# Kernel tuning notes

Measured on AMD Instinct MI355X. Metric: run time of the kernel, lower is better.

Reference implementation:

```python
import jax, jax.numpy as jnp
import numpy as np

B, P, K, F, H = 128, 200, 60, 4, 64   # events, points/event, knn k, feat dim, hidden
N = B * P


def setup_inputs() -> dict:
    key = jax.random.key(0)
    k0, k1, k2, k3 = jax.random.split(key, 4)
    x = jax.random.normal(k0, (N, F), jnp.float32)
    pos = jax.random.normal(k1, (N, 3), jnp.float32)
    batch = jnp.arange(N, dtype=jnp.int32) // P  # sorted event ids, equal-size events
    W1 = jax.random.normal(k2, (F + 3, H), jnp.float32) / np.sqrt(F + 3)
    b1 = jnp.zeros((H,), jnp.float32)
    W2 = jax.random.normal(k3, (H, H), jnp.float32) / np.sqrt(H)
    b2 = jnp.zeros((H,), jnp.float32)
    return {"x": x, "pos": pos, "batch": batch, "W1": W1, "b1": b1, "W2": W2, "b2": b2}


def _knn_edges(pos):
    """knn_graph(pos, K, batch, loop=False, flow='source_to_target').
    Equal-size events -> batched [B,P,P] pairwise distances, no cross-event edges."""
    p = pos.reshape(B, P, 3)
    d2 = jnp.sum((p[:, :, None, :] - p[:, None, :, :]) ** 2, axis=-1)  # [B,P,P]
    d2 = d2 + jnp.eye(P, dtype=d2.dtype) * 1e10                        # exclude self (loop=False)
    _, nbr = jax.lax.top_k(-d2, K)                                     # [B,P,K] local neighbor ids
    src = (nbr + (jnp.arange(B, dtype=nbr.dtype) * P)[:, None, None]).reshape(-1)  # sources j
    dst = jnp.repeat(jnp.arange(N, dtype=src.dtype), K)                             # targets i
    return jnp.stack([src, dst])  # [2, N*K]


def _local_nn(m, W1, b1, W2, b2):
    h = jax.nn.relu(m @ W1 + b1)
    return jax.nn.relu(h @ W2 + b2)


def reference(x, pos, batch, W1, b1, W2, b2):
    edge_index = _knn_edges(pos)
    src, dst = edge_index[0], edge_index[1]
    # PointConv message: net(concat[x_j, pos_j - pos_i]) on each edge
    rel = pos[src] - pos[dst]                             # [E,3]
    m = jnp.concatenate([x[src], rel], axis=-1)           # [E,F+3]
    h = _local_nn(m, W1, b1, W2, b2)                      # [E,H]
    out = h.reshape(N, K, H).max(axis=1)                  # max-aggregate per target node
    # PyG PointConv adds self-loops by default: message with rel = 0
    m_self = jnp.concatenate([x, jnp.zeros((N, 3), x.dtype)], axis=-1)
    h_self = _local_nn(m_self, W1, b1, W2, b2)            # [N,H]
    out = jnp.maximum(out, h_self)
    return (out, pos, batch, edge_index)
```

## Files before the change

### kernel.cpp

```cpp
#include <hip/hip_runtime.h>
#include <hip/hip_bf16.h>

typedef unsigned int u32;
typedef unsigned long long u64;
typedef __attribute__((ext_vector_type(8))) short bf16x8;
typedef __attribute__((ext_vector_type(4))) float f32x4;
typedef __attribute__((ext_vector_type(4))) u32 u32x4;

#define NB 128
#define PP 200
#define KK 60
#define NN (NB*PP)
#define HH 64

#define OUT_OFF   0
#define POS_OFF   (NN*HH)
#define BATCH_OFF (POS_OFF + NN*3)
#define ESRC_OFF  (BATCH_OFF + NN)
#define EDST_OFF  (ESRC_OFF + NN*KK)

static __device__ __forceinline__ u32 packtr(float a, float b) {
    return __builtin_amdgcn_perm(__float_as_uint(b), __float_as_uint(a), 0x07060302u);
}
static __device__ __forceinline__ u32 prefix_lt(u64 b) {
    return __builtin_amdgcn_mbcnt_hi((u32)(b >> 32),
                                     __builtin_amdgcn_mbcnt_lo((u32)b, 0));
}

__global__ __launch_bounds__(256) void fused_kernel(const float* __restrict__ x,
                                                    const float* __restrict__ pos,
                                                    const float* __restrict__ W1,
                                                    const float* __restrict__ b1p,
                                                    const float* __restrict__ W2,
                                                    const float* __restrict__ b2p,
                                                    float* __restrict__ out) {
    __shared__ alignas(16) float xs[PP * 4];
    __shared__ alignas(16) float psl[PP * 3];
    __shared__ alignas(16) u32 jslot[4 * 128];
    __shared__ alignas(16) u32 msg[4 * 256];
    __shared__ alignas(16) u32 pkW1[64 * 4];
    __shared__ alignas(16) u32 pkW2T[64 * 33];
    __shared__ alignas(16) float b2s[64];
    __shared__ alignas(16) u32 zrow[4];

    int tid = threadIdx.x, blk = blockIdx.x;
    int e = blk / 25;
    int pl0b = (blk % 25) * 8;
    int i0b  = e * PP + pl0b;

    if (tid < 200) ((f32x4*)xs)[tid]  = ((const f32x4*)x)[e * PP + tid];
    if (tid < 150) ((f32x4*)psl)[tid] = ((const f32x4*)pos)[e * 150 + tid];
    if (tid < 4)   zrow[tid] = 0u;

    {
        int m = tid & 63, d = tid >> 6;
        float hiv = (d < 3) ? W1[(2*d + 1)*64 + m] : b1p[m];
        pkW1[m*4 + d] = packtr(W1[(2*d)*64 + m], hiv);
    }
    #pragma unroll
    for (int r = 0; r < 8; ++r) {
        int idx = r * 256 + tid;
        int kp = idx >> 6, col = idx & 63;
        pkW2T[col*33 + kp] = packtr(W2[(2*kp)*64 + col], W2[(2*kp + 1)*64 + col]);
    }
    if (tid < 64) b2s[tid] = b2p[tid];
    __syncthreads();

    if (tid < 24) out[POS_OFF + i0b * 3 + tid] = psl[pl0b * 3 + tid];
    if (tid < 8)  out[BATCH_OFF + i0b + tid] = (float)e;

    int lane = tid & 63, wv = tid >> 6;
    int lo16 = lane & 15, hi16 = lane >> 4;
    int plA = pl0b + wv * 2, plB = plA + 1;
    int iA = e * PP + plA,   iB = iA + 1;

    float axA = psl[plA*3], ayA = psl[plA*3+1], azA = psl[plA*3+2];
    float axB = psl[plB*3], ayB = psl[plB*3+1], azB = psl[plB*3+2];

    u32 keyA[4], keyB[4];
    #pragma unroll
    for (int q = 0; q < 4; ++q) {
        int j = lane + q * 64;
        int jc = (j < PP) ? j : 0;
        float px = psl[jc*3], py = psl[jc*3+1], pz = psl[jc*3+2];
        float dxA = px-axA, dyA = py-ayA, dzA = pz-azA;
        float dxB = px-axB, dyB = py-ayB, dzB = pz-azB;
        float d2A = dxA*dxA + dyA*dyA + dzA*dzA;
        float d2B = dxB*dxB + dyB*dyB + dzB*dzB;
        keyA[q] = (j < PP && j != plA)
                ? ((__float_as_uint(d2A) & 0xFFFFFF00u) | (u32)j) : 0xFFFFFFFFu;
        keyB[q] = (j < PP && j != plB)
                ? ((__float_as_uint(d2B) & 0xFFFFFF00u) | (u32)j) : 0xFFFFFFFFu;
    }

    u32 loA = 0u, hiA = 0x7F800000u, loB = 0u, hiB = 0x7F800000u;
    int doneA = 0, doneB = 0;
    #pragma unroll 1
    for (int it = 0; it < 40; ++it) {
        if (!doneA) {
            u32 mA = loA + ((hiA - loA) >> 1);
            int cA = __builtin_popcountll(__ballot(keyA[0] < mA))
                   + __builtin_popcountll(__ballot(keyA[1] < mA))
                   + __builtin_popcountll(__ballot(keyA[2] < mA))
                   + __builtin_popcountll(__ballot(keyA[3] < mA));
            if (cA >= KK) hiA = mA; else loA = mA;
            doneA = (cA == KK) | (hiA - loA <= 1u);
        }
        if (!doneB) {
            u32 mB = loB + ((hiB - loB) >> 1);
            int cB = __builtin_popcountll(__ballot(keyB[0] < mB))
                   + __builtin_popcountll(__ballot(keyB[1] < mB))
                   + __builtin_popcountll(__ballot(keyB[2] < mB))
                   + __builtin_popcountll(__ballot(keyB[3] < mB));
            if (cB >= KK) hiB = mB; else loB = mB;
            doneB = (cB == KK) | (hiB - loB <= 1u);
        }
        if (doneA & doneB) break;
    }

    const int jsb = wv * 128;
    if (lane >= KK) {
        jslot[jsb + lane]      = (u32)plA;
        jslot[jsb + 64 + lane] = (u32)plB;
    }
    #pragma unroll
    for (int t = 0; t < 2; ++t) {
        const u32* key = t ? keyB : keyA;
        u32 hh = t ? hiB : hiA;
        u64 m0 = __ballot(key[0] < hh);
        u64 m1 = __ballot(key[1] < hh);
        u64 m2 = __ballot(key[2] < hh);
        u64 m3 = __ballot(key[3] < hh);
        u32 s1 = (u32)__builtin_popcountll(m0);
        u32 s2 = s1 + (u32)__builtin_popcountll(m1);
        u32 s3 = s2 + (u32)__builtin_popcountll(m2);
        u32 sl[4] = { prefix_lt(m0), s1 + prefix_lt(m1),
                      s2 + prefix_lt(m2), s3 + prefix_lt(m3) };
        #pragma unroll
        for (int q = 0; q < 4; ++q)
            if (key[q] < hh) jslot[jsb + t * 64 + (int)sl[q]] = key[q] & 0xFFu;
    }
    if (lane < KK) {
        out[ESRC_OFF + iA * KK + lane] = (float)(e * PP + (int)jslot[jsb + lane]);
        out[ESRC_OFF + iB * KK + lane] = (float)(e * PP + (int)jslot[jsb + 64 + lane]);
        out[EDST_OFF + iA * KK + lane] = (float)iA;
        out[EDST_OFF + iB * KK + lane] = (float)iB;
    }

    bf16x8 w1f[4];
    #pragma unroll
    for (int th = 0; th < 4; ++th) {
        union { u32 w[4]; bf16x8 v; } u;
        if (hi16 == 0) *(u32x4*)u.w = *(const u32x4*)&pkW1[(th * 16 + lo16) * 4];
        else { u.w[0] = u.w[1] = u.w[2] = u.w[3] = 0u; }
        w1f[th] = u.v;
    }
    bf16x8 bfr[4][2];
    #pragma unroll
    for (int t = 0; t < 4; ++t)
        #pragma unroll
        for (int s = 0; s < 2; ++s) {
            union { u32 w[4]; bf16x8 v; } u;
            int base = (t * 16 + lo16) * 33 + s * 16 + hi16 * 4;
            #pragma unroll
            for (int d = 0; d < 4; ++d) u.w[d] = pkW2T[base + d];
            bfr[t][s] = u.v;
        }
    float b2me = b2s[lane];

    const int msb = wv * 256;
    const u32* mbase = (hi16 == 0) ? &msg[msb + lo16 * 4] : zrow;
    const int mstep  = (hi16 == 0) ? 64 : 0;

    for (int tl = 0; tl < 2; ++tl) {
        int i = iA + tl, pl = plA + tl;
        int jloc = (int)jslot[jsb + tl * 64 + lane];
        f32x4 xv = ((const f32x4*)xs)[jloc];
        float rx = psl[jloc*3]   - psl[pl*3];
        float ry = psl[jloc*3+1] - psl[pl*3+1];
        float rz = psl[jloc*3+2] - psl[pl*3+2];
        u32x4 mrow;
        mrow[0] = packtr(xv[0], xv[1]);
        mrow[1] = packtr(xv[2], xv[3]);
        mrow[2] = packtr(rx, ry);
        mrow[3] = packtr(rz, 1.0f);
        *(u32x4*)&msg[msb + lane * 4] = mrow;

        float rmax[4] = {-3.0e38f, -3.0e38f, -3.0e38f, -3.0e38f};
        #pragma unroll
        for (int rt = 0; rt < 4; ++rt) {
            union { u32 w[4]; bf16x8 v; } mu;
            *(u32x4*)mu.w = *(const u32x4*)(mbase + rt * mstep);

            f32x4 c1[4];
            #pragma unroll
            for (int th = 0; th < 4; ++th)
                c1[th] = __builtin_amdgcn_mfma_f32_16x16x32_bf16(w1f[th], mu.v,
                                                                 (f32x4)0.f, 0, 0, 0);
            f32x4 acc[4];
            #pragma unroll
            for (int t = 0; t < 4; ++t) acc[t] = (f32x4)0.f;

            #pragma unroll
            for (int s = 0; s < 2; ++s) {
                u32 pe0 = packtr(fmaxf(c1[2*s][0], 0.f), fmaxf(c1[2*s][1], 0.f));
                u32 pe1 = packtr(fmaxf(c1[2*s][2], 0.f), fmaxf(c1[2*s][3], 0.f));
                u32 po0 = packtr(fmaxf(c1[2*s+1][0], 0.f), fmaxf(c1[2*s+1][1], 0.f));
                u32 po1 = packtr(fmaxf(c1[2*s+1][2], 0.f), fmaxf(c1[2*s+1][3], 0.f));
                union { u32 w[4]; bf16x8 v; } u;
                {
                    auto t0 = __builtin_amdgcn_permlane32_swap(pe0, po0, false, false);
                    auto w0 = __builtin_amdgcn_permlane16_swap(t0[0], t0[1], false, false);
                    u.w[0] = w0[0]; u.w[2] = w0[1];
                }
                {
                    auto t1 = __builtin_amdgcn_permlane32_swap(pe1, po1, false, false);
                    auto w1 = __builtin_amdgcn_permlane16_swap(t1[0], t1[1], false, false);
                    u.w[1] = w1[0]; u.w[3] = w1[1];
                }
                #pragma unroll
                for (int t = 0; t < 4; ++t)
                    acc[t] = __builtin_amdgcn_mfma_f32_16x16x32_bf16(u.v, bfr[t][s],
                                                                     acc[t], 0, 0, 0);
            }
            #pragma unroll
            for (int t = 0; t < 4; ++t) {
                rmax[t] = fmaxf(fmaxf(acc[t][0], acc[t][1]), rmax[t]);
                rmax[t] = fmaxf(fmaxf(acc[t][2], acc[t][3]), rmax[t]);
            }
        }
        #pragma unroll
        for (int t = 0; t < 4; ++t) {
            rmax[t] = fmaxf(rmax[t], __shfl_xor(rmax[t], 16, 64));
            rmax[t] = fmaxf(rmax[t], __shfl_xor(rmax[t], 32, 64));
        }
        float sel = rmax[0];
        sel = (hi16 == 1) ? rmax[1] : sel;
        sel = (hi16 == 2) ? rmax[2] : sel;
        sel = (hi16 == 3) ? rmax[3] : sel;
        out[OUT_OFF + i * 64 + lane] = fmaxf(sel + b2me, 0.f);
    }
}

extern "C" void kernel_launch(void* const* d_in, const int* in_sizes, int n_in,
                              void* d_out, int out_size, void* d_ws, size_t ws_size,
                              hipStream_t stream) {
    const float* x     = (const float*)d_in[0];
    const float* pos   = (const float*)d_in[1];
    const float* W1    = (const float*)d_in[3];
    const float* b1    = (const float*)d_in[4];
    const float* W2    = (const float*)d_in[5];
    const float* b2    = (const float*)d_in[6];
    float* out = (float*)d_out;
    (void)d_ws; (void)ws_size; (void)in_sizes; (void)n_in; (void)out_size;

    fused_kernel<<<dim3(NN / 8), dim3(256), 0, stream>>>(x, pos, W1, b1, W2, b2, out);
}
```

Before: 110.2 us.

## Process five targets per wave to amortize per-block setup and weight packing

Each wave now handles five target points instead of two, so a block covers 20 points and the grid shrinks from 3200 to 1280 blocks. The per-block work of loading the event's x and pos and packing W1/W2 into shared memory is spread over more points. The bisection top-k is interleaved across five targets, which gives more independent ballots per iteration. W2 packing now uses vectorized float4 loads. The cost is more registers for keys (20 per lane) and fewer blocks, which may lower occupancy and load balance.

```diff
diff --git a/kernel.cpp b/kernel.cpp
--- a/kernel.cpp
+++ b/kernel.cpp
@@ -12,6 +12,9 @@
 #define KK 60
 #define NN (NB*PP)
 #define HH 64
+#define TW 5
+#define TB 20
+#define BPE 10
 
 #define OUT_OFF   0
 #define POS_OFF   (NN*HH)
@@ -36,7 +39,7 @@
                                                     float* __restrict__ out) {
     __shared__ alignas(16) float xs[PP * 4];
     __shared__ alignas(16) float psl[PP * 3];
-    __shared__ alignas(16) u32 jslot[4 * 128];
+    __shared__ alignas(16) u32 jslot[4 * TW * 64];
     __shared__ alignas(16) u32 msg[4 * 256];
     __shared__ alignas(16) u32 pkW1[64 * 4];
     __shared__ alignas(16) u32 pkW2T[64 * 33];
@@ -44,8 +47,8 @@
     __shared__ alignas(16) u32 zrow[4];
 
     int tid = threadIdx.x, blk = blockIdx.x;
-    int e = blk / 25;
-    int pl0b = (blk % 25) * 8;
+    int e = blk / BPE;
+    int pl0b = (blk % BPE) * TB;
     int i0b  = e * PP + pl0b;
 
     if (tid < 200) ((f32x4*)xs)[tid]  = ((const f32x4*)x)[e * PP + tid];
@@ -58,79 +61,79 @@
         pkW1[m*4 + d] = packtr(W1[(2*d)*64 + m], hiv);
     }
     #pragma unroll
-    for (int r = 0; r < 8; ++r) {
-        int idx = r * 256 + tid;
-        int kp = idx >> 6, col = idx & 63;
-        pkW2T[col*33 + kp] = packtr(W2[(2*kp)*64 + col], W2[(2*kp + 1)*64 + col]);
+    for (int r = 0; r < 4; ++r) {
+        int g = r * 256 + tid;
+        int kp = g >> 4, colq = g & 15;
+        f32x4 ra = *(const f32x4*)&W2[(2*kp)    *64 + colq*4];
+        f32x4 rb = *(const f32x4*)&W2[(2*kp + 1)*64 + colq*4];
+        #pragma unroll
+        for (int c = 0; c < 4; ++c)
+            pkW2T[(colq*4 + c)*33 + kp] = packtr(ra[c], rb[c]);
     }
     if (tid < 64) b2s[tid] = b2p[tid];
     __syncthreads();
 
-    if (tid < 24) out[POS_OFF + i0b * 3 + tid] = psl[pl0b * 3 + tid];
-    if (tid < 8)  out[BATCH_OFF + i0b + tid] = (float)e;
+    if (tid < 3*TB) out[POS_OFF + i0b * 3 + tid] = psl[pl0b * 3 + tid];
+    if (tid < TB)   out[BATCH_OFF + i0b + tid] = (float)e;
 
     int lane = tid & 63, wv = tid >> 6;
     int lo16 = lane & 15, hi16 = lane >> 4;
-    int plA = pl0b + wv * 2, plB = plA + 1;
-    int iA = e * PP + plA,   iB = iA + 1;
-
-    float axA = psl[plA*3], ayA = psl[plA*3+1], azA = psl[plA*3+2];
-    float axB = psl[plB*3], ayB = psl[plB*3+1], azB = psl[plB*3+2];
-
-    u32 keyA[4], keyB[4];
-    #pragma unroll
-    for (int q = 0; q < 4; ++q) {
-        int j = lane + q * 64;
-        int jc = (j < PP) ? j : 0;
-        float px = psl[jc*3], py = psl[jc*3+1], pz = psl[jc*3+2];
-        float dxA = px-axA, dyA = py-ayA, dzA = pz-azA;
-        float dxB = px-axB, dyB = py-ayB, dzB = pz-azB;
-        float d2A = dxA*dxA + dyA*dyA + dzA*dzA;
-        float d2B = dxB*dxB + dyB*dyB + dzB*dzB;
-        keyA[q] = (j < PP && j != plA)
-                ? ((__float_as_uint(d2A) & 0xFFFFFF00u) | (u32)j) : 0xFFFFFFFFu;
-        keyB[q] = (j < PP && j != plB)
-                ? ((__float_as_uint(d2B) & 0xFFFFFF00u) | (u32)j) : 0xFFFFFFFFu;
-    }
-
-    u32 loA = 0u, hiA = 0x7F800000u, loB = 0u, hiB = 0x7F800000u;
-    int doneA = 0, doneB = 0;
+    int plW0 = pl0b + wv * TW;
+    int iW0  = e * PP + plW0;
+
+    u32 key[TW][4];
+    {
+        float ax[TW], ay[TW], az[TW];
+        #pragma unroll
+        for (int t = 0; t < TW; ++t) {
+            ax[t] = psl[(plW0+t)*3]; ay[t] = psl[(plW0+t)*3+1]; az[t] = psl[(plW0+t)*3+2];
+        }
+        #pragma unroll
+        for (int q = 0; q < 4; ++q) {
+            int j = lane + q * 64;
+            int jc = (j < PP) ? j : 0;
+            float px = psl[jc*3], py = psl[jc*3+1], pz = psl[jc*3+2];
+            #pragma unroll
+            for (int t = 0; t < TW; ++t) {
+                float dx = px-ax[t], dy = py-ay[t], dz = pz-az[t];
+                float d2 = dx*dx + dy*dy + dz*dz;
+                key[t][q] = (j < PP && j != plW0 + t)
+                          ? ((__float_as_uint(d2) & 0xFFFFFF00u) | (u32)j) : 0xFFFFFFFFu;
+            }
+        }
+    }
+
+    u32 lo[TW], hi[TW]; int done[TW];
+    #pragma unroll
+    for (int t = 0; t < TW; ++t) { lo[t] = 0u; hi[t] = 0x7F800000u; done[t] = 0; }
     #pragma unroll 1
     for (int it = 0; it < 40; ++it) {
-        if (!doneA) {
-            u32 mA = loA + ((hiA - loA) >> 1);
-            int cA = __builtin_popcountll(__ballot(keyA[0] < mA))
-                   + __builtin_popcountll(__ballot(keyA[1] < mA))
-                   + __builtin_popcountll(__ballot(keyA[2] < mA))
-                   + __builtin_popcountll(__ballot(keyA[3] < mA));
-            if (cA >= KK) hiA = mA; else loA = mA;
-            doneA = (cA == KK) | (hiA - loA <= 1u);
-        }
-        if (!doneB) {
-            u32 mB = loB + ((hiB - loB) >> 1);
-            int cB = __builtin_popcountll(__ballot(keyB[0] < mB))
-                   + __builtin_popcountll(__ballot(keyB[1] < mB))
-                   + __builtin_popcountll(__ballot(keyB[2] < mB))
-                   + __builtin_popcountll(__ballot(keyB[3] < mB));
-            if (cB >= KK) hiB = mB; else loB = mB;
-            doneB = (cB == KK) | (hiB - loB <= 1u);
-        }
-        if (doneA & doneB) break;
-    }
-
-    const int jsb = wv * 128;
-    if (lane >= KK) {
-        jslot[jsb + lane]      = (u32)plA;
-        jslot[jsb + 64 + lane] = (u32)plB;
-    }
-    #pragma unroll
-    for (int t = 0; t < 2; ++t) {
-        const u32* key = t ? keyB : keyA;
-        u32 hh = t ? hiB : hiA;
-        u64 m0 = __ballot(key[0] < hh);
-        u64 m1 = __ballot(key[1] < hh);
-        u64 m2 = __ballot(key[2] < hh);
-        u64 m3 = __ballot(key[3] < hh);
+        #pragma unroll
+        for (int t = 0; t < TW; ++t) {
+            if (!done[t]) {
+                u32 m = lo[t] + ((hi[t] - lo[t]) >> 1);
+                int c = __builtin_popcountll(__ballot(key[t][0] < m))
+                      + __builtin_popcountll(__ballot(key[t][1] < m))
+                      + __builtin_popcountll(__ballot(key[t][2] < m))
+                      + __builtin_popcountll(__ballot(key[t][3] < m));
+                if (c >= KK) hi[t] = m; else lo[t] = m;
+                done[t] = (c == KK) | (hi[t] - lo[t] <= 1u);
+            }
+        }
+        int alldone = done[0];
+        #pragma unroll
+        for (int t = 1; t < TW; ++t) alldone &= done[t];
+        if (alldone) break;
+    }
+
+    const int jsb = wv * (TW * 64);
+    #pragma unroll
+    for (int t = 0; t < TW; ++t) {
+        if (lane >= KK) jslot[jsb + t * 64 + lane] = (u32)(plW0 + t);
+        u64 m0 = __ballot(key[t][0] < hi[t]);
+        u64 m1 = __ballot(key[t][1] < hi[t]);
+        u64 m2 = __ballot(key[t][2] < hi[t]);
+        u64 m3 = __ballot(key[t][3] < hi[t]);
         u32 s1 = (u32)__builtin_popcountll(m0);
         u32 s2 = s1 + (u32)__builtin_popcountll(m1);
         u32 s3 = s2 + (u32)__builtin_popcountll(m2);
@@ -138,13 +141,15 @@
                       s2 + prefix_lt(m2), s3 + prefix_lt(m3) };
         #pragma unroll
         for (int q = 0; q < 4; ++q)
-            if (key[q] < hh) jslot[jsb + t * 64 + (int)sl[q]] = key[q] & 0xFFu;
-    }
-    if (lane < KK) {
-        out[ESRC_OFF + iA * KK + lane] = (float)(e * PP + (int)jslot[jsb + lane]);
-        out[ESRC_OFF + iB * KK + lane] = (float)(e * PP + (int)jslot[jsb + 64 + lane]);
-        out[EDST_OFF + iA * KK + lane] = (float)iA;
-        out[EDST_OFF + iB * KK + lane] = (float)iB;
+            if (key[t][q] < hi[t]) jslot[jsb + t * 64 + (int)sl[q]] = key[t][q] & 0xFFu;
+    }
+    #pragma unroll
+    for (int t = 0; t < TW; ++t) {
+        int i = iW0 + t;
+        if (lane < KK) {
+            out[ESRC_OFF + i * KK + lane] = (float)(e * PP + (int)jslot[jsb + t * 64 + lane]);
+            out[EDST_OFF + i * KK + lane] = (float)i;
+        }
     }
 
     bf16x8 w1f[4];
@@ -172,8 +177,8 @@
     const u32* mbase = (hi16 == 0) ? &msg[msb + lo16 * 4] : zrow;
     const int mstep  = (hi16 == 0) ? 64 : 0;
 
-    for (int tl = 0; tl < 2; ++tl) {
-        int i = iA + tl, pl = plA + tl;
+    for (int tl = 0; tl < TW; ++tl) {
+        int i = iW0 + tl, pl = plW0 + tl;
         int jloc = (int)jslot[jsb + tl * 64 + lane];
         f32x4 xv = ((const f32x4*)xs)[jloc];
         float rx = psl[jloc*3]   - psl[pl*3];
@@ -254,5 +259,5 @@
     float* out = (float*)d_out;
     (void)d_ws; (void)ws_size; (void)in_sizes; (void)n_in; (void)out_size;
 
-    fused_kernel<<<dim3(NN / 8), dim3(256), 0, stream>>>(x, pos, W1, b1, W2, b2, out);
-}
+    fused_kernel<<<dim3(NN / TB), dim3(256), 0, stream>>>(x, pos, W1, b1, W2, b2, out);
+}
```

New measurement: 115.3 us. +4.6%, slower.
